# Performance work log

Hardware: AMD Instinct MI355X
Metric: run time of the kernel (lower is better)

Reference implementation:

```python
import jax, jax.numpy as jnp
import numpy as np

B, N, D = 32, 4096, 512
HID = 64
MIN_K, MAX_K = 3, 50
IN_DIM = 3 * D + 5  # mean/max/std pooled features + 5 structural features
NEG_SENTINEL = -1e8


def setup_inputs() -> dict:
    key = jax.random.key(0)
    ks = jax.random.split(key, 9)
    x = jax.random.normal(ks[0], (B, N, D), dtype=jnp.float32)
    keep = jax.random.uniform(ks[1], (B, 1, N)) < 0.75
    mask = jnp.where(keep, 0.0, -1e9).astype(jnp.float32)
    def lin(k, fan_in, fan_out):
        bound = 1.0 / np.sqrt(fan_in)
        kw, kb = jax.random.split(k)
        W = jax.random.uniform(kw, (fan_in, fan_out), minval=-bound, maxval=bound, dtype=jnp.float32)
        b = jax.random.uniform(kb, (fan_out,), minval=-bound, maxval=bound, dtype=jnp.float32)
        return W, b
    W1, b1 = lin(ks[2], IN_DIM, HID)
    W2, b2 = lin(ks[3], HID, HID // 2)
    W3, b3 = lin(ks[4], HID // 2, 1)
    return {"x": x, "mask": mask, "W1": W1, "b1": b1, "W2": W2, "b2": b2, "W3": W3, "b3": b3}


def reference(x, mask, W1, b1, W2, b2, W3, b3):
    valid = mask[:, 0, :] > NEG_SENTINEL            # [B, N] bool
    m = valid.astype(x.dtype)[..., None]            # [B, N, 1]
    cnt = m.sum(axis=1)                             # [B, 1] valid-node counts
    cnt_safe = jnp.maximum(cnt, 1.0)
    has_nodes = cnt > 0.0                           # [B, 1]

    # masked mean / max / unbiased std pooling (segment-reduce over nodes)
    x_mean = (x * m).sum(axis=1) / cnt_safe                                    # [B, D]
    x_mean = jnp.where(has_nodes, x_mean, 0.0)
    x_max = jnp.where(valid[..., None], x, -jnp.inf).max(axis=1)               # [B, D]
    x_max = jnp.where(has_nodes, x_max, 0.0)
    var = (m * (x - x_mean[:, None, :]) ** 2).sum(axis=1) / jnp.maximum(cnt - 1.0, 1.0)
    x_std = jnp.where(has_nodes, jnp.sqrt(var), 0.0)                           # [B, D]

    # structural features: dense path with no edge_index -> constants except log_size
    n = cnt[:, 0]
    log_size = jnp.log(n + 1.0) / 5.0
    ones = jnp.ones_like(log_size)
    # [log_size, density=0.1, avg_degree/10=0.2, max_degree=4.0, degree_std/10=0.1]
    sf = jnp.stack([log_size, 0.1 * ones, 0.2 * ones, 4.0 * ones, 0.1 * ones], axis=1)  # [B, 5]

    g = jnp.concatenate([x_mean, x_max, x_std, sf], axis=1)   # [B, 3D+5]
    h = jax.nn.relu(g @ W1 + b1)                              # dropout is identity in eval
    h = jax.nn.relu(h @ W2 + b2)
    score = jax.nn.sigmoid(h @ W3 + b3)[:, 0]                 # [B]

    num_clusters_cont = MIN_K + score * (MAX_K - MIN_K)
    num_clusters = jnp.round(num_clusters_cont).mean().astype(jnp.int32)
    num_clusters = jnp.clip(num_clusters, MIN_K, MAX_K)
    return num_clusters, score.mean()
```

## Files before the change

kernel.cpp:

```cpp
#include <hip/hip_runtime.h>
#include <cmath>

#define B_      32
#define N_      4096
#define D_      512
#define D4      (D_/4)
#define NCHUNK  32
#define ROWS    (N_/NCHUNK)
#define IN_DIM  1541
#define NEG_SENT (-1.0e8f)

__global__ __launch_bounds__(128) void stats_partial_kernel(
    const float* __restrict__ x, const float* __restrict__ mask,
    float4* __restrict__ psum, float4* __restrict__ psq,
    float4* __restrict__ pmax, float* __restrict__ pcnt)
{
    __shared__ int sidx[ROWS];
    __shared__ int scount;
    const int t = threadIdx.x;
    const int c = blockIdx.x;
    const int b = blockIdx.y;

    if (t == 0) scount = 0;
    __syncthreads();
    {
        const int n = c * ROWS + t;
        const float mv = mask[b * N_ + n];
        if (mv > NEG_SENT) { int p = atomicAdd(&scount, 1); sidx[p] = n; }
    }
    __syncthreads();
    const int m = scount;

    const float4* __restrict__ xb = (const float4*)x + (size_t)b * N_ * D4 + t;

    const float NINF = -__builtin_inff();
    float4 s0 = {0,0,0,0}, s1 = s0, s2 = s0, s3 = s0;
    float4 q0 = s0, q1 = s0, q2 = s0, q3 = s0;
    float4 m0 = {NINF,NINF,NINF,NINF}, m1 = m0, m2 = m0, m3 = m0;

#define ACC(S,Q,M,V) \
    S.x += V.x; S.y += V.y; S.z += V.z; S.w += V.w; \
    Q.x = fmaf(V.x,V.x,Q.x); Q.y = fmaf(V.y,V.y,Q.y); \
    Q.z = fmaf(V.z,V.z,Q.z); Q.w = fmaf(V.w,V.w,Q.w); \
    M.x = fmaxf(M.x,V.x); M.y = fmaxf(M.y,V.y); \
    M.z = fmaxf(M.z,V.z); M.w = fmaxf(M.w,V.w);

    int i = 0;
    for (; i + 4 <= m; i += 4) {
        const int n0 = sidx[i], n1 = sidx[i+1], n2 = sidx[i+2], n3 = sidx[i+3];
        float4 v0 = xb[(size_t)n0 * D4];
        float4 v1 = xb[(size_t)n1 * D4];
        float4 v2 = xb[(size_t)n2 * D4];
        float4 v3 = xb[(size_t)n3 * D4];
        ACC(s0,q0,m0,v0); ACC(s1,q1,m1,v1); ACC(s2,q2,m2,v2); ACC(s3,q3,m3,v3);
    }
    for (; i < m; ++i) {
        float4 v = xb[(size_t)sidx[i] * D4];
        ACC(s0,q0,m0,v);
    }
#undef ACC
    s0.x += s1.x+s2.x+s3.x; s0.y += s1.y+s2.y+s3.y;
    s0.z += s1.z+s2.z+s3.z; s0.w += s1.w+s2.w+s3.w;
    q0.x += q1.x+q2.x+q3.x; q0.y += q1.y+q2.y+q3.y;
    q0.z += q1.z+q2.z+q3.z; q0.w += q1.w+q2.w+q3.w;
    m0.x = fmaxf(fmaxf(m0.x,m1.x), fmaxf(m2.x,m3.x));
    m0.y = fmaxf(fmaxf(m0.y,m1.y), fmaxf(m2.y,m3.y));
    m0.z = fmaxf(fmaxf(m0.z,m1.z), fmaxf(m2.z,m3.z));
    m0.w = fmaxf(fmaxf(m0.w,m1.w), fmaxf(m2.w,m3.w));

    const size_t idx = ((size_t)(b * NCHUNK + c)) * D4 + t;
    psum[idx] = s0; psq[idx] = q0; pmax[idx] = m0;
    if (t == 0) pcnt[b * NCHUNK + c] = (float)m;
}

__global__ __launch_bounds__(128) void mlp_kernel(
    const float4* __restrict__ psum, const float4* __restrict__ psq,
    const float4* __restrict__ pmax, const float* __restrict__ pcnt,
    const float* __restrict__ W1, const float* __restrict__ b1,
    const float* __restrict__ W2, const float* __restrict__ b2,
    const float* __restrict__ W3, const float* __restrict__ b3,
    float* __restrict__ scores)
{
    __shared__ float g[IN_DIM];
    __shared__ float h1[64];
    __shared__ float h2[32];
    const int t = threadIdx.x;
    const int b = blockIdx.x;

    const float NINF = -__builtin_inff();
    float4 s = {0,0,0,0}, q = {0,0,0,0};
    float4 mx = {NINF,NINF,NINF,NINF};
    float cnt = 0.f;
    for (int c = 0; c < NCHUNK; ++c) {
        const size_t idx = ((size_t)(b * NCHUNK + c)) * D4 + t;
        float4 a = psum[idx], u = psq[idx], w = pmax[idx];
        s.x += a.x; s.y += a.y; s.z += a.z; s.w += a.w;
        q.x += u.x; q.y += u.y; q.z += u.z; q.w += u.w;
        mx.x = fmaxf(mx.x,w.x); mx.y = fmaxf(mx.y,w.y);
        mx.z = fmaxf(mx.z,w.z); mx.w = fmaxf(mx.w,w.w);
        cnt += pcnt[b * NCHUNK + c];
    }
    const bool  has = cnt > 0.f;
    const float inv = 1.f / fmaxf(cnt, 1.f);
    const float dn  = 1.f / fmaxf(cnt - 1.f, 1.f);

    float sa[4] = {s.x,s.y,s.z,s.w};
    float qa[4] = {q.x,q.y,q.z,q.w};
    float ma[4] = {mx.x,mx.y,mx.z,mx.w};
    #pragma unroll
    for (int k = 0; k < 4; ++k) {
        const int d = 4*t + k;
        const float mn = has ? sa[k] * inv : 0.f;
        const float vv = fmaxf((qa[k] - cnt * mn * mn) * dn, 0.f);
        g[d]         = mn;
        g[D_ + d]    = has ? ma[k] : 0.f;
        g[2*D_ + d]  = has ? sqrtf(vv) : 0.f;
    }
    if (t == 0) {
        g[3*D_ + 0] = logf(cnt + 1.f) * 0.2f;
        g[3*D_ + 1] = 0.1f;
        g[3*D_ + 2] = 0.2f;
        g[3*D_ + 3] = 4.0f;
        g[3*D_ + 4] = 0.1f;
    }
    __syncthreads();

    if (t < 64) {
        float a0 = b1[t], a1 = 0.f, a2 = 0.f, a3 = 0.f;
        int i = 0;
        for (; i + 4 <= IN_DIM; i += 4) {
            a0 = fmaf(g[i  ], W1[(i  )*64 + t], a0);
            a1 = fmaf(g[i+1], W1[(i+1)*64 + t], a1);
            a2 = fmaf(g[i+2], W1[(i+2)*64 + t], a2);
            a3 = fmaf(g[i+3], W1[(i+3)*64 + t], a3);
        }
        for (; i < IN_DIM; ++i) a0 = fmaf(g[i], W1[i*64 + t], a0);
        h1[t] = fmaxf((a0 + a1) + (a2 + a3), 0.f);
    }
    __syncthreads();

    if (t < 32) {
        float a = b2[t];
        #pragma unroll
        for (int i = 0; i < 64; ++i) a = fmaf(h1[i], W2[i*32 + t], a);
        h2[t] = fmaxf(a, 0.f);
    }
    __syncthreads();

    if (t == 0) {
        float a = b3[0];
        #pragma unroll
        for (int i = 0; i < 32; ++i) a = fmaf(h2[i], W3[i], a);
        scores[b] = 1.f / (1.f + expf(-a));
    }
}

__global__ __launch_bounds__(64) void final_kernel(
    const float* __restrict__ scores, float* __restrict__ out)
{
    const int t = threadIdx.x;
    float sc = (t < B_) ? scores[t] : 0.f;
    float r  = (t < B_) ? rintf(3.f + sc * 47.f) : 0.f;
    #pragma unroll
    for (int off = 32; off > 0; off >>= 1) {
        sc += __shfl_down(sc, off);
        r  += __shfl_down(r,  off);
    }
    if (t == 0) {
        const float mean_r = r * (1.f / 32.f);
        int nc = (int)mean_r;
        nc = nc < 3 ? 3 : (nc > 50 ? 50 : nc);
        out[0] = (float)nc;
        out[1] = sc * (1.f / 32.f);
    }
}

extern "C" void kernel_launch(void* const* d_in, const int* in_sizes, int n_in,
                              void* d_out, int out_size, void* d_ws, size_t ws_size,
                              hipStream_t stream)
{
    const float* x    = (const float*)d_in[0];
    const float* mask = (const float*)d_in[1];
    const float* W1   = (const float*)d_in[2];
    const float* b1   = (const float*)d_in[3];
    const float* W2   = (const float*)d_in[4];
    const float* b2   = (const float*)d_in[5];
    const float* W3   = (const float*)d_in[6];
    const float* b3   = (const float*)d_in[7];
    float* out = (float*)d_out;

    const size_t PCOUNT = (size_t)B_ * NCHUNK * D4;
    float4* psum = (float4*)d_ws;
    float4* psq  = psum + PCOUNT;
    float4* pmax = psq  + PCOUNT;
    float*  pcnt = (float*)(pmax + PCOUNT);
    float*  scores = pcnt + (size_t)B_ * NCHUNK;

    dim3 gridA(NCHUNK, B_);
    stats_partial_kernel<<<gridA, 128, 0, stream>>>(x, mask, psum, psq, pmax, pcnt);
    mlp_kernel<<<B_, 128, 0, stream>>>(psum, psq, pmax, pcnt,
                                       W1, b1, W2, b2, W3, b3, scores);
    final_kernel<<<1, 64, 0, stream>>>(scores, out);
}
```

Baseline: 404.1 us.

## Replace compacted gather with dense masked streaming and split MLP work

The stats kernel stops compacting valid row indices into shared memory. It now streams every row of each 64-row chunk with unrolled, independent loads and applies the mask arithmetically: a 0/1 weight for sum and sum-of-squares, and a large negative offset for max. The grid doubles to 64 chunks per batch, and the MLP kernel uses 256 threads to split both the partial reduction and the W1 dot product. The goal is more memory-level parallelism and no index indirection, at the cost of also reading padded rows.

```diff
diff --git a/kernel.cpp b/kernel.cpp
--- a/kernel.cpp
+++ b/kernel.cpp
@@ -5,60 +5,69 @@
 #define N_      4096
 #define D_      512
 #define D4      (D_/4)
-#define NCHUNK  32
-#define ROWS    (N_/NCHUNK)
+#define NCH     64
+#define RPC     64
 #define IN_DIM  1541
 #define NEG_SENT (-1.0e8f)
-
-__global__ __launch_bounds__(128) void stats_partial_kernel(
+#define BIGNEG   (1.0e30f)
+
+__global__ __launch_bounds__(128, 4) void stats_partial_kernel(
     const float* __restrict__ x, const float* __restrict__ mask,
     float4* __restrict__ psum, float4* __restrict__ psq,
     float4* __restrict__ pmax, float* __restrict__ pcnt)
 {
-    __shared__ int sidx[ROWS];
-    __shared__ int scount;
-    const int t = threadIdx.x;
-    const int c = blockIdx.x;
-    const int b = blockIdx.y;
-
-    if (t == 0) scount = 0;
-    __syncthreads();
-    {
-        const int n = c * ROWS + t;
-        const float mv = mask[b * N_ + n];
-        if (mv > NEG_SENT) { int p = atomicAdd(&scount, 1); sidx[p] = n; }
-    }
-    __syncthreads();
-    const int m = scount;
-
-    const float4* __restrict__ xb = (const float4*)x + (size_t)b * N_ * D4 + t;
-
-    const float NINF = -__builtin_inff();
+    __shared__ float sw[RPC];
+    __shared__ float so[RPC];
+    const int tx = threadIdx.x;
+    const int c  = blockIdx.x;
+    const int b  = blockIdx.y;
+
+    if (tx < RPC) {
+        const float mv = mask[b * N_ + c * RPC + tx];
+        const float w  = (mv > NEG_SENT) ? 1.f : 0.f;
+        sw[tx] = w;
+        so[tx] = (w - 1.f) * BIGNEG;
+    }
+    __syncthreads();
+
+    const float4* __restrict__ xb =
+        (const float4*)x + ((size_t)b * N_ + (size_t)c * RPC) * D4 + tx;
+
     float4 s0 = {0,0,0,0}, s1 = s0, s2 = s0, s3 = s0;
     float4 q0 = s0, q1 = s0, q2 = s0, q3 = s0;
-    float4 m0 = {NINF,NINF,NINF,NINF}, m1 = m0, m2 = m0, m3 = m0;
-
-#define ACC(S,Q,M,V) \
-    S.x += V.x; S.y += V.y; S.z += V.z; S.w += V.w; \
-    Q.x = fmaf(V.x,V.x,Q.x); Q.y = fmaf(V.y,V.y,Q.y); \
-    Q.z = fmaf(V.z,V.z,Q.z); Q.w = fmaf(V.w,V.w,Q.w); \
-    M.x = fmaxf(M.x,V.x); M.y = fmaxf(M.y,V.y); \
-    M.z = fmaxf(M.z,V.z); M.w = fmaxf(M.w,V.w);
-
-    int i = 0;
-    for (; i + 4 <= m; i += 4) {
-        const int n0 = sidx[i], n1 = sidx[i+1], n2 = sidx[i+2], n3 = sidx[i+3];
-        float4 v0 = xb[(size_t)n0 * D4];
-        float4 v1 = xb[(size_t)n1 * D4];
-        float4 v2 = xb[(size_t)n2 * D4];
-        float4 v3 = xb[(size_t)n3 * D4];
-        ACC(s0,q0,m0,v0); ACC(s1,q1,m1,v1); ACC(s2,q2,m2,v2); ACC(s3,q3,m3,v3);
-    }
-    for (; i < m; ++i) {
-        float4 v = xb[(size_t)sidx[i] * D4];
-        ACC(s0,q0,m0,v);
+    float4 m0 = {-BIGNEG,-BIGNEG,-BIGNEG,-BIGNEG}, m1 = m0, m2 = m0, m3 = m0;
+
+#define ACC(S,Q,M,V,W,O) { \
+    float tvx = (V).x*(W), tvy = (V).y*(W), tvz = (V).z*(W), tvw = (V).w*(W); \
+    (S).x += tvx; (S).y += tvy; (S).z += tvz; (S).w += tvw; \
+    (Q).x = fmaf(tvx,(V).x,(Q).x); (Q).y = fmaf(tvy,(V).y,(Q).y); \
+    (Q).z = fmaf(tvz,(V).z,(Q).z); (Q).w = fmaf(tvw,(V).w,(Q).w); \
+    (M).x = fmaxf((M).x, fmaf((W),(V).x,(O))); \
+    (M).y = fmaxf((M).y, fmaf((W),(V).y,(O))); \
+    (M).z = fmaxf((M).z, fmaf((W),(V).z,(O))); \
+    (M).w = fmaxf((M).w, fmaf((W),(V).w,(O))); }
+
+    #pragma unroll
+    for (int j = 0; j < RPC; j += 8) {
+        float4 v0 = xb[(size_t)(j+0) * D4];
+        float4 v1 = xb[(size_t)(j+1) * D4];
+        float4 v2 = xb[(size_t)(j+2) * D4];
+        float4 v3 = xb[(size_t)(j+3) * D4];
+        float4 v4 = xb[(size_t)(j+4) * D4];
+        float4 v5 = xb[(size_t)(j+5) * D4];
+        float4 v6 = xb[(size_t)(j+6) * D4];
+        float4 v7 = xb[(size_t)(j+7) * D4];
+        ACC(s0,q0,m0,v0, sw[j+0], so[j+0]);
+        ACC(s1,q1,m1,v1, sw[j+1], so[j+1]);
+        ACC(s2,q2,m2,v2, sw[j+2], so[j+2]);
+        ACC(s3,q3,m3,v3, sw[j+3], so[j+3]);
+        ACC(s0,q0,m0,v4, sw[j+4], so[j+4]);
+        ACC(s1,q1,m1,v5, sw[j+5], so[j+5]);
+        ACC(s2,q2,m2,v6, sw[j+6], so[j+6]);
+        ACC(s3,q3,m3,v7, sw[j+7], so[j+7]);
     }
 #undef ACC
+
     s0.x += s1.x+s2.x+s3.x; s0.y += s1.y+s2.y+s3.y;
     s0.z += s1.z+s2.z+s3.z; s0.w += s1.w+s2.w+s3.w;
     q0.x += q1.x+q2.x+q3.x; q0.y += q1.y+q2.y+q3.y;
@@ -68,12 +77,18 @@
     m0.z = fmaxf(fmaxf(m0.z,m1.z), fmaxf(m2.z,m3.z));
     m0.w = fmaxf(fmaxf(m0.w,m1.w), fmaxf(m2.w,m3.w));
 
-    const size_t idx = ((size_t)(b * NCHUNK + c)) * D4 + t;
+    const size_t idx = ((size_t)(b * NCH + c)) * D4 + tx;
     psum[idx] = s0; psq[idx] = q0; pmax[idx] = m0;
-    if (t == 0) pcnt[b * NCHUNK + c] = (float)m;
-}
-
-__global__ __launch_bounds__(128) void mlp_kernel(
+
+    if (tx == 0) {
+        float cv = 0.f;
+        #pragma unroll
+        for (int j = 0; j < RPC; ++j) cv += sw[j];
+        pcnt[b * NCH + c] = cv;
+    }
+}
+
+__global__ __launch_bounds__(256) void mlp_kernel(
     const float4* __restrict__ psum, const float4* __restrict__ psq,
     const float4* __restrict__ pmax, const float* __restrict__ pcnt,
     const float* __restrict__ W1, const float* __restrict__ b1,
@@ -81,73 +96,99 @@
     const float* __restrict__ W3, const float* __restrict__ b3,
     float* __restrict__ scores)
 {
+    __shared__ float4 Ss[2][D4], Sq[2][D4], Sm[2][D4];
     __shared__ float g[IN_DIM];
+    __shared__ float h1p[4*64];
     __shared__ float h1[64];
     __shared__ float h2[32];
-    const int t = threadIdx.x;
-    const int b = blockIdx.x;
-
-    const float NINF = -__builtin_inff();
-    float4 s = {0,0,0,0}, q = {0,0,0,0};
-    float4 mx = {NINF,NINF,NINF,NINF};
-    float cnt = 0.f;
-    for (int c = 0; c < NCHUNK; ++c) {
-        const size_t idx = ((size_t)(b * NCHUNK + c)) * D4 + t;
-        float4 a = psum[idx], u = psq[idx], w = pmax[idx];
-        s.x += a.x; s.y += a.y; s.z += a.z; s.w += a.w;
-        q.x += u.x; q.y += u.y; q.z += u.z; q.w += u.w;
-        mx.x = fmaxf(mx.x,w.x); mx.y = fmaxf(mx.y,w.y);
-        mx.z = fmaxf(mx.z,w.z); mx.w = fmaxf(mx.w,w.w);
-        cnt += pcnt[b * NCHUNK + c];
-    }
-    const bool  has = cnt > 0.f;
-    const float inv = 1.f / fmaxf(cnt, 1.f);
-    const float dn  = 1.f / fmaxf(cnt - 1.f, 1.f);
-
-    float sa[4] = {s.x,s.y,s.z,s.w};
-    float qa[4] = {q.x,q.y,q.z,q.w};
-    float ma[4] = {mx.x,mx.y,mx.z,mx.w};
-    #pragma unroll
-    for (int k = 0; k < 4; ++k) {
-        const int d = 4*t + k;
-        const float mn = has ? sa[k] * inv : 0.f;
-        const float vv = fmaxf((qa[k] - cnt * mn * mn) * dn, 0.f);
-        g[d]         = mn;
-        g[D_ + d]    = has ? ma[k] : 0.f;
-        g[2*D_ + d]  = has ? sqrtf(vv) : 0.f;
-    }
-    if (t == 0) {
-        g[3*D_ + 0] = logf(cnt + 1.f) * 0.2f;
-        g[3*D_ + 1] = 0.1f;
-        g[3*D_ + 2] = 0.2f;
-        g[3*D_ + 3] = 4.0f;
-        g[3*D_ + 4] = 0.1f;
-    }
-    __syncthreads();
-
-    if (t < 64) {
-        float a0 = b1[t], a1 = 0.f, a2 = 0.f, a3 = 0.f;
-        int i = 0;
-        for (; i + 4 <= IN_DIM; i += 4) {
-            a0 = fmaf(g[i  ], W1[(i  )*64 + t], a0);
-            a1 = fmaf(g[i+1], W1[(i+1)*64 + t], a1);
-            a2 = fmaf(g[i+2], W1[(i+2)*64 + t], a2);
-            a3 = fmaf(g[i+3], W1[(i+3)*64 + t], a3);
+    __shared__ float scnt;
+
+    const int tid = threadIdx.x;
+    const int tx  = tid & 127;
+    const int ty  = tid >> 7;
+    const int b   = blockIdx.x;
+
+    {
+        float4 s = {0,0,0,0}, q = {0,0,0,0};
+        float4 mx = {-BIGNEG,-BIGNEG,-BIGNEG,-BIGNEG};
+        const int c0 = ty * (NCH/2);
+        for (int c = c0; c < c0 + NCH/2; ++c) {
+            const size_t idx = ((size_t)(b * NCH + c)) * D4 + tx;
+            float4 a = psum[idx], u = psq[idx], w = pmax[idx];
+            s.x += a.x; s.y += a.y; s.z += a.z; s.w += a.w;
+            q.x += u.x; q.y += u.y; q.z += u.z; q.w += u.w;
+            mx.x = fmaxf(mx.x,w.x); mx.y = fmaxf(mx.y,w.y);
+            mx.z = fmaxf(mx.z,w.z); mx.w = fmaxf(mx.w,w.w);
         }
-        for (; i < IN_DIM; ++i) a0 = fmaf(g[i], W1[i*64 + t], a0);
-        h1[t] = fmaxf((a0 + a1) + (a2 + a3), 0.f);
-    }
-    __syncthreads();
-
-    if (t < 32) {
-        float a = b2[t];
-        #pragma unroll
-        for (int i = 0; i < 64; ++i) a = fmaf(h1[i], W2[i*32 + t], a);
-        h2[t] = fmaxf(a, 0.f);
-    }
-    __syncthreads();
-
-    if (t == 0) {
+        Ss[ty][tx] = s; Sq[ty][tx] = q; Sm[ty][tx] = mx;
+    }
+    if (tid < 64) {
+        float cv = pcnt[b * NCH + tid];
+        #pragma unroll
+        for (int off = 32; off > 0; off >>= 1) cv += __shfl_down(cv, off);
+        if (tid == 0) scnt = cv;
+    }
+    __syncthreads();
+
+    const float cnt = scnt;
+    if (ty == 0) {
+        float4 s = Ss[0][tx], s_ = Ss[1][tx];
+        float4 q = Sq[0][tx], q_ = Sq[1][tx];
+        float4 mx = Sm[0][tx], m_ = Sm[1][tx];
+        s.x += s_.x; s.y += s_.y; s.z += s_.z; s.w += s_.w;
+        q.x += q_.x; q.y += q_.y; q.z += q_.z; q.w += q_.w;
+        mx.x = fmaxf(mx.x,m_.x); mx.y = fmaxf(mx.y,m_.y);
+        mx.z = fmaxf(mx.z,m_.z); mx.w = fmaxf(mx.w,m_.w);
+
+        const bool  has = cnt > 0.f;
+        const float inv = 1.f / fmaxf(cnt, 1.f);
+        const float dn  = 1.f / fmaxf(cnt - 1.f, 1.f);
+        float sa[4] = {s.x,s.y,s.z,s.w};
+        float qa[4] = {q.x,q.y,q.z,q.w};
+        float ma[4] = {mx.x,mx.y,mx.z,mx.w};
+        #pragma unroll
+        for (int k = 0; k < 4; ++k) {
+            const int d = 4*tx + k;
+            const float mn = has ? sa[k] * inv : 0.f;
+            const float vv = fmaxf((qa[k] - cnt * mn * mn) * dn, 0.f);
+            g[d]        = mn;
+            g[D_ + d]   = has ? ma[k] : 0.f;
+            g[2*D_ + d] = has ? sqrtf(vv) : 0.f;
+        }
+        if (tx == 0) {
+            g[3*D_ + 0] = logf(cnt + 1.f) * 0.2f;
+            g[3*D_ + 1] = 0.1f;
+            g[3*D_ + 2] = 0.2f;
+            g[3*D_ + 3] = 4.0f;
+            g[3*D_ + 4] = 0.1f;
+        }
+    }
+    __syncthreads();
+
+    {
+        const int o   = tid & 63;
+        const int grp = tid >> 6;
+        float a = 0.f;
+        for (int i = grp; i < IN_DIM; i += 4)
+            a = fmaf(g[i], W1[i*64 + o], a);
+        h1p[tid] = a;
+    }
+    __syncthreads();
+    if (tid < 64) {
+        float a = b1[tid] + ((h1p[tid] + h1p[64+tid]) + (h1p[128+tid] + h1p[192+tid]));
+        h1[tid] = fmaxf(a, 0.f);
+    }
+    __syncthreads();
+
+    if (tid < 32) {
+        float a = b2[tid];
+        #pragma unroll
+        for (int i = 0; i < 64; ++i) a = fmaf(h1[i], W2[i*32 + tid], a);
+        h2[tid] = fmaxf(a, 0.f);
+    }
+    __syncthreads();
+
+    if (tid == 0) {
         float a = b3[0];
         #pragma unroll
         for (int i = 0; i < 32; ++i) a = fmaf(h2[i], W3[i], a);
@@ -189,16 +230,16 @@
     const float* b3   = (const float*)d_in[7];
     float* out = (float*)d_out;
 
-    const size_t PCOUNT = (size_t)B_ * NCHUNK * D4;
+    const size_t PCOUNT = (size_t)B_ * NCH * D4;
     float4* psum = (float4*)d_ws;
     float4* psq  = psum + PCOUNT;
     float4* pmax = psq  + PCOUNT;
     float*  pcnt = (float*)(pmax + PCOUNT);
-    float*  scores = pcnt + (size_t)B_ * NCHUNK;
-
-    dim3 gridA(NCHUNK, B_);
+    float*  scores = pcnt + (size_t)B_ * NCH;
+
+    dim3 gridA(NCH, B_);
     stats_partial_kernel<<<gridA, 128, 0, stream>>>(x, mask, psum, psq, pmax, pcnt);
-    mlp_kernel<<<B_, 128, 0, stream>>>(psum, psq, pmax, pcnt,
+    mlp_kernel<<<B_, 256, 0, stream>>>(psum, psq, pmax, pcnt,
                                        W1, b1, W2, b2, W3, b3, scores);
     final_kernel<<<1, 64, 0, stream>>>(scores, out);
 }
```

Measured after the change: 587.2 us. 1.45x slower.
